# Optimization experiments

Hardware: AMD Instinct MI355X
Metric: run time of the kernel (lower is better)

## Reference

```python
import jax, jax.numpy as jnp
import numpy as np

NV = 8192   # number of nodes
NE = 8192   # number of edges
IN_V = 512
OUT_V = 512
IN_E = 512
A_COEF = 0.5  # self.a ; self.b = 1 - a


def setup_inputs() -> dict:
    key = jax.random.key(0)
    k = jax.random.split(key, 8)
    stdv = 1.0 / np.sqrt(OUT_V)
    return {
        "H_v": jax.random.normal(k[0], (NV, IN_V), dtype=jnp.float32),
        "H_e": jax.random.normal(k[1], (NE, IN_E), dtype=jnp.float32),
        "adj_e": jax.random.uniform(k[2], (NE, NE), dtype=jnp.float32),
        "adj_v": jax.random.uniform(k[3], (NV, NV), dtype=jnp.float32),
        "T": jax.random.uniform(k[4], (NV, NE), dtype=jnp.float32),
        "weight": jax.random.uniform(k[5], (IN_V, OUT_V), minval=-stdv, maxval=stdv, dtype=jnp.float32),
        "p": jax.random.normal(k[6], (1, IN_E), dtype=jnp.float32),
        "bias": jax.random.uniform(k[7], (OUT_V,), minval=-stdv, maxval=stdv, dtype=jnp.float32),
    }


def reference(H_v, H_e, adj_e, adj_v, T, weight, p, bias):
    # node_layer=True path of GraphConvolution.forward
    # gate: per-edge scalar from H_e @ p^T  -> [Ne]
    gate = (H_e @ p.T)[:, 0]
    # T @ diag(gate) @ T^T computed as broadcast column-scale (same math,
    # avoids materializing the Ne x Ne diagonal)
    multiplier1 = (T * gate[None, :]) @ T.T            # [Nv, Nv]
    eye = jnp.eye(multiplier1.shape[0], dtype=multiplier1.dtype)
    M1 = eye + (1.0 - eye) * multiplier1
    adjusted_A = M1 * adj_v
    H_v_weight = H_v @ weight                          # [Nv, out_v]
    output = adjusted_A @ H_v_weight
    output1 = adj_v @ H_v_weight
    output = output * A_COEF + output1 * (1.0 - A_COEF)
    ret = output + bias
    return (ret, H_e)
```

## Files before the change

kernel.cpp:

```cpp
#include <hip/hip_runtime.h>
#include <hip/hip_bf16.h>

typedef __attribute__((ext_vector_type(4))) float  f32x4;
typedef __attribute__((ext_vector_type(8))) short  s16x8;
typedef __attribute__((ext_vector_type(4))) short  s16x4;

#define NV 8192
#define NE 8192
#define DIM 512

__device__ inline short f2bf(float x) {
    unsigned u = __float_as_uint(x);
    u += 0x7fffu + ((u >> 16) & 1u);
    return (short)(u >> 16);
}
__device__ inline float bf2f(short s) {
    return __uint_as_float(((unsigned)(unsigned short)s) << 16);
}

__global__ void gate_kernel(const float* __restrict__ He, const float* __restrict__ p,
                            float* __restrict__ gate) {
    int row  = blockIdx.x * 4 + (threadIdx.x >> 6);
    int lane = threadIdx.x & 63;
    const float* r = He + (size_t)row * DIM + lane * 8;
    float4 a0 = *(const float4*)r;
    float4 a1 = *(const float4*)(r + 4);
    float4 p0 = *(const float4*)(p + lane * 8);
    float4 p1 = *(const float4*)(p + lane * 8 + 4);
    float s = a0.x*p0.x + a0.y*p0.y + a0.z*p0.z + a0.w*p0.w
            + a1.x*p1.x + a1.y*p1.y + a1.z*p1.z + a1.w*p1.w;
    #pragma unroll
    for (int off = 32; off; off >>= 1) s += __shfl_down(s, off);
    if (lane == 0) gate[row] = s;
}

__global__ void convert_T(const float* __restrict__ T, const float* __restrict__ gate,
                          short* __restrict__ Tg, short* __restrict__ Tb) {
    size_t gid  = (size_t)blockIdx.x * blockDim.x + threadIdx.x;
    size_t base = gid * 8;
    int col = (int)(base & (NE - 1));
    float4 t0 = *(const float4*)(T + base);
    float4 t1 = *(const float4*)(T + base + 4);
    float4 g0 = *(const float4*)(gate + col);
    float4 g1 = *(const float4*)(gate + col + 4);
    s16x8 vb, vg;
    vb[0]=f2bf(t0.x); vb[1]=f2bf(t0.y); vb[2]=f2bf(t0.z); vb[3]=f2bf(t0.w);
    vb[4]=f2bf(t1.x); vb[5]=f2bf(t1.y); vb[6]=f2bf(t1.z); vb[7]=f2bf(t1.w);
    vg[0]=f2bf(t0.x*g0.x); vg[1]=f2bf(t0.y*g0.y); vg[2]=f2bf(t0.z*g0.z); vg[3]=f2bf(t0.w*g0.w);
    vg[4]=f2bf(t1.x*g1.x); vg[5]=f2bf(t1.y*g1.y); vg[6]=f2bf(t1.z*g1.z); vg[7]=f2bf(t1.w*g1.w);
    *(s16x8*)(Tb + base) = vb;
    *(s16x8*)(Tg + base) = vg;
}

__global__ void to_bf16(const float* __restrict__ in, short* __restrict__ out) {
    size_t base = ((size_t)blockIdx.x * blockDim.x + threadIdx.x) * 8;
    float4 a = *(const float4*)(in + base);
    float4 b = *(const float4*)(in + base + 4);
    s16x8 v;
    v[0]=f2bf(a.x); v[1]=f2bf(a.y); v[2]=f2bf(a.z); v[3]=f2bf(a.w);
    v[4]=f2bf(b.x); v[5]=f2bf(b.y); v[6]=f2bf(b.z); v[7]=f2bf(b.w);
    *(s16x8*)(out + base) = v;
}

__global__ void wT_bf16(const float* __restrict__ W, short* __restrict__ WT) {
    __shared__ short t[64][65];
    int rb = blockIdx.x, cb = blockIdx.y;
    int c = threadIdx.x & 63, r0 = threadIdx.x >> 6;
    #pragma unroll
    for (int i = 0; i < 16; ++i) {
        int r = i * 4 + r0;
        t[r][c] = f2bf(W[(size_t)(rb * 64 + r) * DIM + cb * 64 + c]);
    }
    __syncthreads();
    #pragma unroll
    for (int i = 0; i < 16; ++i) {
        int r = i * 4 + r0;
        WT[(size_t)(cb * 64 + r) * DIM + rb * 64 + c] = t[c][r];
    }
}

template<int EPI>
__global__ __launch_bounds__(256)
void gemm_bt(const short* __restrict__ A, const short* __restrict__ B,
             int M, int N, int K,
             short* __restrict__ Cb,
             const float* __restrict__ bias, float* __restrict__ Cf) {
    __shared__ short As[128 * 32];
    __shared__ short Bs[128 * 32];

    int nwg = gridDim.x;
    int bid = blockIdx.x;
    int cpx = nwg >> 3;
    bid = (bid & 7) * cpx + (bid >> 3);

    const int nbn = N >> 7;
    const int bm = (bid / nbn) << 7;
    const int bn = (bid % nbn) << 7;
    const int tid  = threadIdx.x;
    const int lane = tid & 63;
    const int wave = tid >> 6;
    const int wrow = (wave >> 1) * 64;
    const int wcol = (wave & 1) * 64;

    f32x4 acc[4][4] = {};

    const int lrow = lane >> 2;
    const int lcol = ((lane & 3) ^ ((lrow >> 1) & 3)) * 8;

    for (int k0 = 0; k0 < K; k0 += 32) {
        #pragma unroll
        for (int it = 0; it < 2; ++it) {
            int chunk = it * 4 + wave;
            int row = chunk * 16 + lrow;
            __builtin_amdgcn_global_load_lds(
                (const __attribute__((address_space(1))) void*)(A + (size_t)(bm + row) * K + k0 + lcol),
                (__attribute__((address_space(3))) void*)(As + chunk * 512), 16, 0, 0);
            __builtin_amdgcn_global_load_lds(
                (const __attribute__((address_space(1))) void*)(B + (size_t)(bn + row) * K + k0 + lcol),
                (__attribute__((address_space(3))) void*)(Bs + chunk * 512), 16, 0, 0);
        }
        __syncthreads();

        const int fr = lane & 15;
        const int sw = (fr >> 1) & 3;
        const int sa = ((lane >> 4) ^ sw) * 8;
        s16x8 af[4], bfr[4];
        #pragma unroll
        for (int i = 0; i < 4; ++i) {
            af[i]  = *(const s16x8*)&As[(wrow + i * 16 + fr) * 32 + sa];
            bfr[i] = *(const s16x8*)&Bs[(wcol + i * 16 + fr) * 32 + sa];
        }
        #pragma unroll
        for (int i = 0; i < 4; ++i)
            #pragma unroll
            for (int j = 0; j < 4; ++j)
                acc[i][j] = __builtin_amdgcn_mfma_f32_16x16x32_bf16(af[i], bfr[j], acc[i][j], 0, 0, 0);
        __syncthreads();
    }

    const int fr = lane & 15, fq = (lane >> 4) * 4;
    #pragma unroll
    for (int i = 0; i < 4; ++i) {
        #pragma unroll
        for (int j = 0; j < 4; ++j) {
            int col = bn + wcol + j * 16 + fr;
            #pragma unroll
            for (int v = 0; v < 4; ++v) {
                int row = bm + wrow + i * 16 + fq + v;
                float d = acc[i][j][v];
                if (EPI == 1) Cf[(size_t)row * N + col] = d + bias[col];
                else          Cb[(size_t)row * N + col] = f2bf(d);
            }
        }
    }
}

#define FENCE asm volatile("" ::: "memory")
#define BAR   do { FENCE; __builtin_amdgcn_s_barrier(); FENCE; } while (0)
#define MFMA16(I0, J0)                                                                       \
    _Pragma("unroll") for (int x = 0; x < 4; ++x)                                            \
    _Pragma("unroll") for (int y = 0; y < 2; ++y)                                            \
    _Pragma("unroll") for (int s = 0; s < 2; ++s)                                            \
        acc[(I0)+x][(J0)+y] = __builtin_amdgcn_mfma_f32_16x16x32_bf16(                       \
            af[x][s], bf[(J0)+y][s], acc[(I0)+x][(J0)+y], 0, 0, 0);

#define GEMM256_CORE(NIT, KMASK)                                                             \
    stageA(0, 0, 0); stageA(0, 1, 0);                                                        \
    stageB(0, 0, 0); stageB(0, 1, 0);                                                        \
    stageB(1, 0, 1); stageB(1, 1, 1);                                                        \
    asm volatile("s_waitcnt vmcnt(4)" ::: "memory");                                         \
    __builtin_amdgcn_s_barrier();                                                            \
    FENCE;                                                                                   \
    _Pragma("unroll 1")                                                                      \
    for (int it = 0; it < (NIT); ++it) {                                                     \
        const int kt = it * 2;                                                               \
        _Pragma("unroll") for (int x = 0; x < 4; ++x) { af[x][0] = lda(A0o, x, 0); af[x][1] = lda(A0o, x, 1); } \
        _Pragma("unroll") for (int y = 0; y < 2; ++y) { bf[y][0] = ldb(B0o, y, 0); bf[y][1] = ldb(B0o, y, 1); } \
        stageA(1, 0, kt + 1);                                                                \
        asm volatile("s_waitcnt lgkmcnt(8)" ::: "memory");                                   \
        BAR; __builtin_amdgcn_s_setprio(1); MFMA16(0, 0) __builtin_amdgcn_s_setprio(0); BAR; \
        _Pragma("unroll") for (int y = 0; y < 2; ++y) { bf[2+y][0] = ldb(B0o, 2+y, 0); bf[2+y][1] = ldb(B0o, 2+y, 1); } \
        stageA(1, 1, kt + 1);                                                                \
        BAR; __builtin_amdgcn_s_setprio(1); MFMA16(0, 2) __builtin_amdgcn_s_setprio(0); BAR; \
        _Pragma("unroll") for (int x = 0; x < 4; ++x) { af[x][0] = lda(A0o, 4+x, 0); af[x][1] = lda(A0o, 4+x, 1); } \
        stageB(0, 0, kt + 2);                                                                \
        BAR; __builtin_amdgcn_s_setprio(1); MFMA16(4, 0) __builtin_amdgcn_s_setprio(0); BAR; \
        stageB(0, 1, kt + 2);                                                                \
        BAR; __builtin_amdgcn_s_setprio(1); MFMA16(4, 2) __builtin_amdgcn_s_setprio(0);      \
        asm volatile("s_waitcnt vmcnt(4)" ::: "memory"); BAR;                                \
        _Pragma("unroll") for (int x = 0; x < 4; ++x) { af[x][0] = lda(A1o, x, 0); af[x][1] = lda(A1o, x, 1); } \
        _Pragma("unroll") for (int y = 0; y < 2; ++y) { bf[y][0] = ldb(B1o, y, 0); bf[y][1] = ldb(B1o, y, 1); } \
        stageA(0, 0, kt + 2);                                                                \
        asm volatile("s_waitcnt lgkmcnt(8)" ::: "memory");                                   \
        BAR; __builtin_amdgcn_s_setprio(1); MFMA16(0, 0) __builtin_amdgcn_s_setprio(0); BAR; \
        _Pragma("unroll") for (int y = 0; y < 2; ++y) { bf[2+y][0] = ldb(B1o, 2+y, 0); bf[2+y][1] = ldb(B1o, 2+y, 1); } \
        stageA(0, 1, kt + 2);                                                                \
        BAR; __builtin_amdgcn_s_setprio(1); MFMA16(0, 2) __builtin_amdgcn_s_setprio(0); BAR; \
        _Pragma("unroll") for (int x = 0; x < 4; ++x) { af[x][0] = lda(A1o, 4+x, 0); af[x][1] = lda(A1o, 4+x, 1); } \
        stageB(1, 0, kt + 3);                                                                \
        BAR; __builtin_amdgcn_s_setprio(1); MFMA16(4, 0) __builtin_amdgcn_s_setprio(0); BAR; \
        stageB(1, 1, kt + 3);                                                                \
        BAR; __builtin_amdgcn_s_setprio(1); MFMA16(4, 2) __builtin_amdgcn_s_setprio(0);      \
        asm volatile("s_waitcnt vmcnt(4)" ::: "memory"); BAR;                                \
    }                                                                                        \
    asm volatile("s_waitcnt vmcnt(0)" ::: "memory");                                         \
    BAR;

#define GEMM256_PRELUDE(KMASK)                                                               \
    const int tid  = threadIdx.x;                                                            \
    const int wave = tid >> 6;                                                               \
    const int lane = tid & 63;                                                               \
    const int wm = wave >> 2;                                                                \
    const int wn = wave & 3;                                                                 \
    const int fr = lane & 15;                                                                \
    const int kq = lane >> 4;                                                                \
    const int lr = lane >> 3;                                                                \
    const int lsl = (lane & 7) ^ lr;                                                         \
    const int A0o = wm * 8192;                                                               \
    const int A1o = 16384 + wm * 8192;                                                       \
    const int B0o = 32768 + ((wn >> 1) << 13);                                               \
    const int B1o = B0o + 16384;                                                             \
    const short* aSrc = A + (size_t)(bm + wave * 8 + lr) * 8192 + kb + lsl * 8;              \
    const short* bSrc = B + (size_t)(bn + wave * 8 + lr) * 8192 + kb + lsl * 8;              \
    auto stageA = [&](int buf, int h, int kt) {                                              \
        const short* s0 = aSrc + ((size_t)h << 20) + ((kt << 6) & (KMASK));                  \
        short* d = &lds[buf * 16384 + h * 8192 + wave * 512];                                \
        __builtin_amdgcn_global_load_lds((const __attribute__((address_space(1))) void*)s0,  \
            (__attribute__((address_space(3))) void*)d, 16, 0, 0);                           \
        __builtin_amdgcn_global_load_lds((const __attribute__((address_space(1))) void*)(s0 + (size_t)(64 * 8192)), \
            (__attribute__((address_space(3))) void*)(d + 4096), 16, 0, 0);                  \
    };                                                                                       \
    auto stageB = [&](int buf, int h, int kt) {                                              \
        const short* s0 = bSrc + ((size_t)h << 20) + ((kt << 6) & (KMASK));                  \
        short* d = &lds[32768 + buf * 16384 + h * 8192 + wave * 512];                        \
        __builtin_amdgcn_global_load_lds((const __attribute__((address_space(1))) void*)s0,  \
            (__attribute__((address_space(3))) void*)d, 16, 0, 0);                           \
        __builtin_amdgcn_global_load_lds((const __attribute__((address_space(1))) void*)(s0 + (size_t)(64 * 8192)), \
            (__attribute__((address_space(3))) void*)(d + 4096), 16, 0, 0);                  \
    };                                                                                       \
    auto lda = [&](int base, int i, int ks) -> s16x8 {                                       \
        int rl = i * 16 + fr;                                                                \
        int slot = ((ks << 2) + kq) ^ (rl & 7);                                              \
        return *(const s16x8*)&lds[base + rl * 64 + slot * 8];                               \
    };                                                                                       \
    auto ldb = [&](int base, int j, int ks) -> s16x8 {                                       \
        int rl = ((wn & 1) << 6) + j * 16 + fr;                                              \
        int slot = ((ks << 2) + kq) ^ (rl & 7);                                              \
        return *(const s16x8*)&lds[base + rl * 64 + slot * 8];                               \
    };                                                                                       \
    f32x4 acc[8][4] = {};                                                                    \
    s16x8 af[4][2], bf[4][2];

__global__ __launch_bounds__(512, 2)
void gemm256(const short* __restrict__ A, const short* __restrict__ B,
             const float* __restrict__ adj, short* __restrict__ Cb) {
    __shared__ short lds[65536];

    int b = blockIdx.x;
    b = (b & 7) * 64 + (b >> 3);
    int bi, bj;
    if (b < 496) {
        int rem = b;
        bi = 0;
        while (rem >= 31 - bi) { rem -= 31 - bi; ++bi; }
        bj = bi + 1 + rem;
    } else {
        bi = bj = b - 496;
    }
    const int bm = bi << 8;
    const int bn = bj << 8;
    const int kb = 0;

    GEMM256_PRELUDE(8191)
    GEMM256_CORE(64, 8191)

    const int fq = kq << 2;
    #pragma unroll
    for (int i = 0; i < 8; ++i) {
        int rl0 = wm * 128 + i * 16 + fq;
        #pragma unroll
        for (int j = 0; j < 4; ++j) {
            int cl = wn * 64 + j * 16 + fr;
            #pragma unroll
            for (int v = 0; v < 4; ++v) {
                int rl = rl0 + v;
                lds[rl * 256 + (cl ^ ((rl & 7) << 3))] = f2bf(acc[i][j][v]);
            }
        }
    }
    BAR;

    const int rloc = tid >> 5;
    const int cc   = (tid & 31) * 8;
    #pragma unroll 4
    for (int m = 0; m < 16; ++m) {
        int r = m * 16 + rloc;
        s16x8 mv = *(const s16x8*)&lds[r * 256 + (cc ^ ((r & 7) << 3))];
        const float* arow = adj + (size_t)(bm + r) * 8192 + bn + cc;
        float4 a0 = *(const float4*)arow;
        float4 a1 = *(const float4*)(arow + 4);
        float av[8] = {a0.x,a0.y,a0.z,a0.w,a1.x,a1.y,a1.z,a1.w};
        s16x8 o;
        #pragma unroll
        for (int e = 0; e < 8; ++e) {
            float cv = av[e] * (0.5f * bf2f(mv[e]) + 0.5f);
            if (bm == bn && r == cc + e) cv = av[e];
            o[e] = f2bf(cv);
        }
        *(s16x8*)&Cb[(size_t)(bm + r) * 8192 + bn + cc] = o;
    }

    if (bm != bn) {
        #pragma unroll 1
        for (int h = 0; h < 2; ++h) {
            BAR;
            if ((wn >> 1) == h) {
                #pragma unroll
                for (int i = 0; i < 8; ++i) {
                    #pragma unroll
                    for (int j = 0; j < 4; ++j) {
                        int c = ((wn & 1) << 6) + j * 16 + fr;
                        #pragma unroll
                        for (int v = 0; v < 4; ++v) {
                            int r = wm * 128 + i * 16 + fq + v;
                            lds[c * 264 + r] = f2bf(acc[i][j][v]);
                        }
                    }
                }
            }
            BAR;
            const int r0 = (tid & 31) * 8;
            #pragma unroll 2
            for (int itr = 0; itr < 8; ++itr) {
                int c = itr * 16 + (tid >> 5);
                s16x8 mv = *(const s16x8*)&lds[c * 264 + r0];
                const float* arow = adj + (size_t)(bn + h * 128 + c) * 8192 + bm + r0;
                float4 a0 = *(const float4*)arow;
                float4 a1 = *(const float4*)(arow + 4);
                float av[8] = {a0.x,a0.y,a0.z,a0.w,a1.x,a1.y,a1.z,a1.w};
                s16x8 o;
                #pragma unroll
                for (int e = 0; e < 8; ++e)
                    o[e] = f2bf(av[e] * (0.5f * bf2f(mv[e]) + 0.5f));
                *(s16x8*)&Cb[(size_t)(bn + h * 128 + c) * 8192 + bm + r0] = o;
            }
        }
    }
}

__global__ __launch_bounds__(512, 2)
void gemm256_ks(const short* __restrict__ A, const short* __restrict__ B,
                float* __restrict__ part) {
    __shared__ short lds[65536];

    int b = blockIdx.x;
    const int t  = b >> 4;
    const int ks = b & 15;
    const int bm = (16 + t) << 8;
    const int bn = bm;
    const int kb = ks << 9;

    GEMM256_PRELUDE(511)
    GEMM256_CORE(4, 511)

    float* po = part + (size_t)(t * 16 + ks) * 65536;
    const int fq = kq << 2;
    #pragma unroll
    for (int i = 0; i < 8; ++i) {
        #pragma unroll
        for (int j = 0; j < 4; ++j) {
            int C = wn * 64 + j * 16 + fr;
            #pragma unroll
            for (int v = 0; v < 4; ++v) {
                int R = wm * 128 + i * 16 + fq + v;
                po[R * 256 + C] = acc[i][j][v];
            }
        }
    }
}

__global__ void reduce_diag(const float* __restrict__ part, const float* __restrict__ adj,
                            short* __restrict__ Cb) {
    int b = blockIdx.x;
    int t = b >> 5, sub = b & 31;
    int base = sub * 2048 + threadIdx.x * 8;
    int r = base >> 8, c = base & 255;
    const float* ps = part + (size_t)t * 16 * 65536 + base;
    float s[8] = {};
    #pragma unroll
    for (int ks = 0; ks < 16; ++ks) {
        f32x4 a = *(const f32x4*)(ps + (size_t)ks * 65536);
        f32x4 bq = *(const f32x4*)(ps + (size_t)ks * 65536 + 4);
        s[0]+=a[0]; s[1]+=a[1]; s[2]+=a[2]; s[3]+=a[3];
        s[4]+=bq[0]; s[5]+=bq[1]; s[6]+=bq[2]; s[7]+=bq[3];
    }
    int gr = (16 + t) * 256 + r, gc0 = (16 + t) * 256 + c;
    const float* arow = adj + (size_t)gr * 8192 + gc0;
    float4 a0 = *(const float4*)arow, a1 = *(const float4*)(arow + 4);
    float av[8] = {a0.x,a0.y,a0.z,a0.w,a1.x,a1.y,a1.z,a1.w};
    s16x8 o;
    #pragma unroll
    for (int e = 0; e < 8; ++e) {
        float cv = av[e] * (0.5f * s[e] + 0.5f);
        if (gr == gc0 + e) cv = av[e];
        o[e] = f2bf(cv);
    }
    *(s16x8*)&Cb[(size_t)gr * 8192 + gc0] = o;
}

extern "C" void kernel_launch(void* const* d_in, const int* in_sizes, int n_in,
                              void* d_out, int out_size, void* d_ws, size_t ws_size,
                              hipStream_t stream) {
    const float* Hv   = (const float*)d_in[0];
    const float* He   = (const float*)d_in[1];
    const float* adjv = (const float*)d_in[3];
    const float* T    = (const float*)d_in[4];
    const float* Wf   = (const float*)d_in[5];
    const float* p    = (const float*)d_in[6];
    const float* bias = (const float*)d_in[7];
    float* out = (float*)d_out;

    char* ws = (char*)d_ws;
    float* gate = (float*)(ws);
    short* Hvb  = (short*)(ws + 32768);
    short* Wt   = (short*)(ws + 8421376);
    short* Tg   = (short*)(ws + 16809984);
    short* Tb   = (short*)(ws + 151027712);
    short* Cb   = (short*)(ws + 285245440);
    short* WTb  = (short*)(ws + 285245440);
    float* part = (float*)(ws + 16809984);

    hipMemcpyAsync(out + (size_t)NV * DIM, He, (size_t)NE * DIM * sizeof(float),
                   hipMemcpyDeviceToDevice, stream);

    gate_kernel<<<NE / 4, 256, 0, stream>>>(He, p, gate);
    convert_T<<<(NV * (NE / 8)) / 256, 256, 0, stream>>>(T, gate, Tg, Tb);
    to_bf16<<<(NV * DIM / 8) / 256, 256, 0, stream>>>(Hv, Hvb);
    wT_bf16<<<dim3(8, 8), 256, 0, stream>>>(Wf, WTb);

    gemm_bt<2><<<(DIM / 128) * (NV / 128), 256, 0, stream>>>(
        WTb, Hvb, DIM, NV, DIM, Wt, nullptr, nullptr);

    gemm256<<<512, 512, 0, stream>>>(Tg, Tb, adjv, Cb);
    gemm256_ks<<<256, 512, 0, stream>>>(Tg, Tb, part);
    reduce_diag<<<512, 256, 0, stream>>>(part, adjv, Cb);

    gemm_bt<1><<<(NV / 128) * (DIM / 128), 256, 0, stream>>>(
        Cb, Wt, NV, DIM, NV, nullptr, bias, out);
}
```

Baseline: 835.2 us.

## Replace final GEMM with split-K 256-tile kernel plus bias reduction

The final Cb @ Wt GEMM, previously a 128-tile gemm_bt over 256 blocks, now uses the 256x256 tiled core with a 4-way K split. Partial sums go to workspace and a separate reduce kernel adds them with the bias. This targets better per-tile reuse and more parallelism on the long K=8192 reduction, at the cost of writing and re-reading fp32 partials plus an extra launch. It also packs the LDS stores in the epilogue of the earlier GEMM into 4-wide vector writes.

```diff
diff --git a/kernel.cpp b/kernel.cpp
--- a/kernel.cpp
+++ b/kernel.cpp
@@ -317,14 +317,14 @@
             if ((wn >> 1) == h) {
                 #pragma unroll
                 for (int i = 0; i < 8; ++i) {
+                    int r0 = wm * 128 + i * 16 + fq;
                     #pragma unroll
                     for (int j = 0; j < 4; ++j) {
                         int c = ((wn & 1) << 6) + j * 16 + fr;
-                        #pragma unroll
-                        for (int v = 0; v < 4; ++v) {
-                            int r = wm * 128 + i * 16 + fq + v;
-                            lds[c * 264 + r] = f2bf(acc[i][j][v]);
-                        }
+                        s16x4 o4;
+                        o4[0] = f2bf(acc[i][j][0]); o4[1] = f2bf(acc[i][j][1]);
+                        o4[2] = f2bf(acc[i][j][2]); o4[3] = f2bf(acc[i][j][3]);
+                        *(s16x4*)&lds[c * 264 + r0] = o4;
                     }
                 }
             }
@@ -408,6 +408,64 @@
     *(s16x8*)&Cb[(size_t)gr * 8192 + gc0] = o;
 }
 
+__global__ __launch_bounds__(512, 2)
+void gemm_fin(const short* __restrict__ A, const short* __restrict__ B,
+              float* __restrict__ part) {
+    __shared__ short lds[65536];
+
+    int b = blockIdx.x;
+    const int ks  = b & 3;
+    const int bmi = (b >> 2) & 31;
+    const int bni = b >> 7;
+    const int bm = bmi << 8;
+    const int bn = bni << 8;
+    const int kb = ks << 11;
+
+    GEMM256_PRELUDE(2047)
+    GEMM256_CORE(16, 2047)
+
+    float* po = part + ((size_t)(bmi * 2 + bni) * 4 + ks) * 65536;
+    const int fq = kq << 2;
+    #pragma unroll
+    for (int i = 0; i < 8; ++i) {
+        #pragma unroll
+        for (int j = 0; j < 4; ++j) {
+            int C = wn * 64 + j * 16 + fr;
+            #pragma unroll
+            for (int v = 0; v < 4; ++v) {
+                int R = wm * 128 + i * 16 + fq + v;
+                po[R * 256 + C] = acc[i][j][v];
+            }
+        }
+    }
+}
+
+__global__ void reduce_out(const float* __restrict__ part, const float* __restrict__ bias,
+                           float* __restrict__ out) {
+    size_t g = ((size_t)blockIdx.x * 256 + threadIdx.x) * 8;
+    int r = (int)(g >> 9);
+    int c = (int)(g & 511);
+    int tile = ((r >> 8) << 1) + (c >> 8);
+    size_t inner = (size_t)(r & 255) * 256 + (c & 255);
+    const float* ps = part + ((size_t)tile * 4) * 65536 + inner;
+    float s[8] = {};
+    #pragma unroll
+    for (int ks = 0; ks < 4; ++ks) {
+        f32x4 a = *(const f32x4*)(ps + (size_t)ks * 65536);
+        f32x4 bq = *(const f32x4*)(ps + (size_t)ks * 65536 + 4);
+        s[0]+=a[0]; s[1]+=a[1]; s[2]+=a[2]; s[3]+=a[3];
+        s[4]+=bq[0]; s[5]+=bq[1]; s[6]+=bq[2]; s[7]+=bq[3];
+    }
+    float4 b0 = *(const float4*)(bias + c);
+    float4 b1 = *(const float4*)(bias + c + 4);
+    float bv[8] = {b0.x,b0.y,b0.z,b0.w,b1.x,b1.y,b1.z,b1.w};
+    f32x4 o0, o1;
+    o0[0]=s[0]+bv[0]; o0[1]=s[1]+bv[1]; o0[2]=s[2]+bv[2]; o0[3]=s[3]+bv[3];
+    o1[0]=s[4]+bv[4]; o1[1]=s[5]+bv[5]; o1[2]=s[6]+bv[6]; o1[3]=s[7]+bv[7];
+    *(f32x4*)(out + g) = o0;
+    *(f32x4*)(out + g + 4) = o1;
+}
+
 extern "C" void kernel_launch(void* const* d_in, const int* in_sizes, int n_in,
                               void* d_out, int out_size, void* d_ws, size_t ws_size,
                               hipStream_t stream) {
@@ -429,6 +487,7 @@
     short* Cb   = (short*)(ws + 285245440);
     short* WTb  = (short*)(ws + 285245440);
     float* part = (float*)(ws + 16809984);
+    float* part2 = (float*)(ws + 16809984);
 
     hipMemcpyAsync(out + (size_t)NV * DIM, He, (size_t)NE * DIM * sizeof(float),
                    hipMemcpyDeviceToDevice, stream);
@@ -445,6 +504,6 @@
     gemm256_ks<<<256, 512, 0, stream>>>(Tg, Tb, part);
     reduce_diag<<<512, 256, 0, stream>>>(part, adjv, Cb);
 
-    gemm_bt<1><<<(NV / 128) * (DIM / 128), 256, 0, stream>>>(
-        Cb, Wt, NV, DIM, NV, nullptr, bias, out);
-}
+    gemm_fin<<<256, 512, 0, stream>>>(Cb, Wt, part2);
+    reduce_out<<<(NV * DIM / 8) / 256, 256, 0, stream>>>(part2, bias, out);
+}
```

After: 725.9 us (median of 3 runs). 13.1% less time.
